# Performance work log

Measured on AMD Instinct MI355X. Metric: run time of the kernel, lower is better.

The kernel has to match this reference:

```python
import jax, jax.numpy as jnp
import numpy as np

EPS = 1e-5
B, C_IN, T_IN = 512, 12, 5000
NF, HID, LAT = 32, 64, 32


def setup_inputs() -> dict:
    key = jax.random.key(0)
    ks = jax.random.split(key, 12)
    inp = {
        "x": jax.random.normal(ks[0], (B, C_IN, T_IN), dtype=jnp.float32),
        # conv stack
        "conv1_w": jax.random.normal(ks[1], (32, C_IN, 50), dtype=jnp.float32) * 0.05,
        "conv1_b": jnp.zeros((32,), dtype=jnp.float32),
        "bn1_g": jnp.ones((32,), dtype=jnp.float32),
        "bn1_b": jnp.zeros((32,), dtype=jnp.float32),
        "conv2_w": jax.random.normal(ks[2], (NF, 32, 25), dtype=jnp.float32) * 0.05,
        "conv2_b": jnp.zeros((NF,), dtype=jnp.float32),
        "bn2_g": jnp.ones((NF,), dtype=jnp.float32),
        "bn2_b": jnp.zeros((NF,), dtype=jnp.float32),
        # input projection + layernorm
        "proj_w": jax.random.normal(ks[3], (LAT, NF), dtype=jnp.float32) * 0.1,
        "proj_b": jnp.zeros((LAT,), dtype=jnp.float32),
        "ln_g": jnp.ones((LAT,), dtype=jnp.float32),
        "ln_b": jnp.zeros((LAT,), dtype=jnp.float32),
        # PLRNN recurrence params
        "A": jnp.eye(LAT, dtype=jnp.float32) * 0.9,
        "W": jax.random.normal(ks[4], (LAT, HID), dtype=jnp.float32) * 0.1,
        "h_bias": jnp.zeros((HID,), dtype=jnp.float32),
        # output projection
        "out_w": jax.random.normal(ks[5], (LAT, LAT), dtype=jnp.float32) * 0.1,
        "out_b": jnp.zeros((LAT,), dtype=jnp.float32),
    }
    return inp


def _conv1d(x, w, b, stride):
    # x: [B, C, T], w: [O, I, K]
    y = jax.lax.conv_general_dilated(
        x, w, window_strides=(stride,), padding="VALID",
        dimension_numbers=("NCH", "OIH", "NCH"))
    return y + b[None, :, None]


def _batchnorm_train(x, g, b):
    # training-mode BN over (batch, time) per channel; x: [B, C, T]
    mean = jnp.mean(x, axis=(0, 2), keepdims=True)
    var = jnp.mean((x - mean) ** 2, axis=(0, 2), keepdims=True)
    return (x - mean) * jax.lax.rsqrt(var + EPS) * g[None, :, None] + b[None, :, None]


def _layernorm(x, g, b):
    mean = jnp.mean(x, axis=-1, keepdims=True)
    var = jnp.mean((x - mean) ** 2, axis=-1, keepdims=True)
    return (x - mean) * jax.lax.rsqrt(var + EPS) * g + b


def reference(x, conv1_w, conv1_b, bn1_g, bn1_b, conv2_w, conv2_b, bn2_g, bn2_b,
              proj_w, proj_b, ln_g, ln_b, A, W, h_bias, out_w, out_b):
    # conv front-end
    y = jax.nn.relu(_batchnorm_train(_conv1d(x, conv1_w, conv1_b, 10), bn1_g, bn1_b))
    y = jax.nn.relu(_batchnorm_train(_conv1d(y, conv2_w, conv2_b, 5), bn2_g, bn2_b))
    y = jnp.transpose(y, (0, 2, 1))  # [B, T, NF], T = 95

    # input projection + LN, vectorized over all timesteps
    xt = _layernorm(jnp.einsum("btf,lf->btl", y, proj_w) + proj_b, ln_g, ln_b)  # [B, T, L]
    xs = jnp.transpose(xt, (1, 0, 2))  # [T, B, L] for scan

    def step(h, x_t):
        # h: [B, L]
        linear = h @ A.T
        nonlinear = jax.nn.relu(h @ W + h_bias) @ W.T
        h_new = linear + nonlinear + x_t
        return h_new, h_new

    h0 = jnp.zeros((x.shape[0], A.shape[0]), dtype=x.dtype)
    _, outputs = jax.lax.scan(step, h0, xs)  # [T, B, L]

    pooled = jnp.mean(outputs, axis=0)  # [B, L]
    return pooled @ out_w.T + out_b
```

## Files before the change

kernel.cpp:

```cpp
#include <hip/hip_runtime.h>

#define NB    512
#define CIN   12
#define TIN   5000
#define C1    32
#define T1    496
#define T2    95
#define LATD  32
#define HIDD  64

#define OFS_STATS 0
#define OFS_W1P   256
#define OFS_W2P   19456
#define OFS_Y1    45056
#define OFS_Y2    8171520
#define OFS_XS    OFS_Y1

__global__ void prep_kernel(const float* __restrict__ w1, const float* __restrict__ w2,
                            float* __restrict__ ws) {
    int idx = blockIdx.x * 256 + threadIdx.x;
    if (idx < 256) ws[idx] = 0.f;
    int j = idx - 256;
    if (j >= 0 && j < 19200) {
        int ic = j / 1600, r = j % 1600, k = r / 32, oc = r % 32;
        ws[OFS_W1P + j] = w1[oc * 600 + ic * 50 + k];
    }
    int j2 = idx - 19456;
    if (j2 >= 0 && j2 < 25600) {
        int ic = j2 / 800, r = j2 % 800, k = r / 32, oc = r % 32;
        ws[OFS_W2P + j2] = w2[oc * 800 + ic * 25 + k];
    }
}

__global__ __launch_bounds__(128, 2) void conv1_kernel(const float* __restrict__ x,
                                                       const float* __restrict__ b1,
                                                       float* __restrict__ ws) {
    const float* w1p = ws + OFS_W1P;
    float* y1 = ws + OFS_Y1;
    float* stats = ws + OFS_STATS;
    int b  = blockIdx.x >> 1;
    int t0 = (blockIdx.x & 1) * 256;
    int tid = threadIdx.x;
    int ocg = tid & 3, tg = tid >> 2;
    int oc0 = ocg * 8, lt0 = tg * 8;
    int xbase = 82 * tg;

    __shared__ __align__(16) float xs_s[2][2664];
    __shared__ __align__(16) float ws_s[2][1600];
    __shared__ float sred[128];

    float acc[8][8];
#pragma unroll
    for (int a = 0; a < 8; ++a)
#pragma unroll
        for (int c = 0; c < 8; ++c) acc[a][c] = 0.f;

    const float* xb = x + (size_t)b * (CIN * TIN) + t0 * 10;
    int nvalid = TIN - t0 * 10;

    float4 px[6];
    float4 pw[4];

    auto fetch = [&](int ic) {
#pragma unroll
        for (int j = 0; j < 6; ++j) {
            int i = tid + j * 128;
            if (i < 650) {
                int src = 4 * i;
                const float* gp = xb + ic * TIN + src;
                float4 v;
                if (src + 4 <= nvalid) {
                    v = *(const float4*)gp;
                } else {
                    v.x = (src + 0 < nvalid) ? gp[0] : 0.f;
                    v.y = (src + 1 < nvalid) ? gp[1] : 0.f;
                    v.z = (src + 2 < nvalid) ? gp[2] : 0.f;
                    v.w = (src + 3 < nvalid) ? gp[3] : 0.f;
                }
                px[j] = v;
            }
        }
#pragma unroll
        for (int j = 0; j < 4; ++j) {
            int i = tid + j * 128;
            if (i < 400) pw[j] = *(const float4*)(w1p + ic * 1600 + 4 * i);
        }
    };

    fetch(0);
    for (int ic = 0; ic < CIN; ++ic) {
        int cur = ic & 1;
        __syncthreads();
#pragma unroll
        for (int j = 0; j < 6; ++j) {
            int i = tid + j * 128;
            if (i < 650) {
                int src = 4 * i;
                int dst = src + (i / 20) * 2;
                float2 lo; lo.x = px[j].x; lo.y = px[j].y;
                float2 hi; hi.x = px[j].z; hi.y = px[j].w;
                *(float2*)&xs_s[cur][dst]     = lo;
                *(float2*)&xs_s[cur][dst + 2] = hi;
            }
        }
#pragma unroll
        for (int j = 0; j < 4; ++j) {
            int i = tid + j * 128;
            if (i < 400) *(float4*)&ws_s[cur][4 * i] = pw[j];
        }
        if (ic + 1 < CIN) fetch(ic + 1);
        __syncthreads();

#pragma unroll 1
        for (int kp = 0; kp < 25; ++kp) {
            const int k = kp * 2;
            const float* wr = &ws_s[cur][k * 32 + oc0];
            float4 w00 = *(const float4*)wr;
            float4 w01 = *(const float4*)(wr + 4);
            float4 w10 = *(const float4*)(wr + 32);
            float4 w11 = *(const float4*)(wr + 36);
            float2 xv[8];
#pragma unroll
            for (int jt = 0; jt < 8; ++jt) {
                int r = jt * 10 + k;
                int ad = xbase + r + ((r >= 80) ? 2 : 0);
                xv[jt] = *(const float2*)&xs_s[cur][ad];
            }
            float wk[8]  = {w00.x, w00.y, w00.z, w00.w, w01.x, w01.y, w01.z, w01.w};
            float wk1[8] = {w10.x, w10.y, w10.z, w10.w, w11.x, w11.y, w11.z, w11.w};
#pragma unroll
            for (int jo = 0; jo < 8; ++jo)
#pragma unroll
                for (int jt = 0; jt < 8; ++jt)
                    acc[jo][jt] = fmaf(wk1[jo], xv[jt].y, fmaf(wk[jo], xv[jt].x, acc[jo][jt]));
        }
    }

    float bias[8];
#pragma unroll
    for (int jo = 0; jo < 8; ++jo) bias[jo] = b1[oc0 + jo];

    bool tvalid = (t0 + lt0) <= (T1 - 8);
    float psum[8], psq[8];
#pragma unroll
    for (int jo = 0; jo < 8; ++jo) {
        float s = 0.f, q = 0.f;
        if (tvalid) {
            float tmp[8];
#pragma unroll
            for (int jt = 0; jt < 8; ++jt) {
                float v = acc[jo][jt] + bias[jo];
                tmp[jt] = v; s += v; q = fmaf(v, v, q);
            }
            float* yrow = y1 + (size_t)(b * 32 + oc0 + jo) * T1 + t0 + lt0;
            float4 o0; o0.x = tmp[0]; o0.y = tmp[1]; o0.z = tmp[2]; o0.w = tmp[3];
            float4 o1; o1.x = tmp[4]; o1.y = tmp[5]; o1.z = tmp[6]; o1.w = tmp[7];
            *(float4*)yrow       = o0;
            *(float4*)(yrow + 4) = o1;
        }
        psum[jo] = s; psq[jo] = q;
    }
#pragma unroll
    for (int off = 32; off >= 4; off >>= 1) {
#pragma unroll
        for (int jo = 0; jo < 8; ++jo) {
            psum[jo] += __shfl_down(psum[jo], off, 64);
            psq[jo]  += __shfl_down(psq[jo],  off, 64);
        }
    }
    int lane = tid & 63, wvi = tid >> 6;
    if (lane < 4) {
#pragma unroll
        for (int jo = 0; jo < 8; ++jo) {
            sred[((wvi * 4 + lane) * 8 + jo) * 2 + 0] = psum[jo];
            sred[((wvi * 4 + lane) * 8 + jo) * 2 + 1] = psq[jo];
        }
    }
    __syncthreads();
    if (tid < 64) {
        int oc = tid >> 1, which = tid & 1;
        int og = oc >> 3, jo = oc & 7;
        float v = sred[((0 * 4 + og) * 8 + jo) * 2 + which] +
                  sred[((1 * 4 + og) * 8 + jo) * 2 + which];
        atomicAdd(&stats[which * 32 + oc], v);
    }
}

__global__ void bnstats_kernel(const float* __restrict__ g, const float* __restrict__ bparm,
                               float* __restrict__ ws, int base_in, int base_out, float invN) {
    int oc = threadIdx.x;
    if (oc < 32) {
        float* stats = ws + OFS_STATS;
        float mean = stats[base_in + oc] * invN;
        float var  = stats[base_in + 32 + oc] * invN - mean * mean;
        float s = g[oc] * rsqrtf(var + 1e-5f);
        stats[base_out + oc]      = s;
        stats[base_out + 32 + oc] = bparm[oc] - mean * s;
    }
}

__global__ __launch_bounds__(192, 2) void conv2_kernel(const float* __restrict__ b2,
                                                       float* __restrict__ ws) {
    const float* w2p = ws + OFS_W2P;
    const float* y1 = ws + OFS_Y1;
    float* y2 = ws + OFS_Y2;
    float* stats = ws + OFS_STATS;
    int b = blockIdx.x;
    int tid = threadIdx.x;
    int ocg = tid & 7, tg = tid >> 3;
    int oc0 = ocg * 4, lt0 = tg * 4;

    __shared__ __align__(16) float a1s[500];
    __shared__ __align__(16) float w2s[800];
    __shared__ float sred[192];

    float acc[4][4];
#pragma unroll
    for (int a = 0; a < 4; ++a)
#pragma unroll
        for (int c = 0; c < 4; ++c) acc[a][c] = 0.f;

    for (int ic = 0; ic < 32; ++ic) {
        __syncthreads();
        float s1  = stats[128 + ic];
        float sh1 = stats[160 + ic];
        const float* yrow = y1 + (size_t)(b * 32 + ic) * T1;
        for (int i = tid; i < 124; i += 192) {
            float4 v = *(const float4*)(yrow + 4 * i);
            v.x = fmaxf(fmaf(v.x, s1, sh1), 0.f);
            v.y = fmaxf(fmaf(v.y, s1, sh1), 0.f);
            v.z = fmaxf(fmaf(v.z, s1, sh1), 0.f);
            v.w = fmaxf(fmaf(v.w, s1, sh1), 0.f);
            *(float4*)&a1s[4 * i] = v;
        }
        for (int i = tid; i < 200; i += 192)
            *(float4*)&w2s[4 * i] = *(const float4*)(w2p + ic * 800 + 4 * i);
        __syncthreads();

#pragma unroll 1
        for (int kp = 0; kp < 12; ++kp) {
            const int k = kp * 2;
            float4 wA = *(const float4*)&w2s[k * 32 + oc0];
            float4 wB = *(const float4*)&w2s[(k + 1) * 32 + oc0];
            float x0[4], x1[4];
#pragma unroll
            for (int jt = 0; jt < 4; ++jt) {
                int a = 20 * tg + 5 * jt + k;
                x0[jt] = a1s[a]; x1[jt] = a1s[a + 1];
            }
            float wk[4]  = {wA.x, wA.y, wA.z, wA.w};
            float wk1[4] = {wB.x, wB.y, wB.z, wB.w};
#pragma unroll
            for (int jo = 0; jo < 4; ++jo)
#pragma unroll
                for (int jt = 0; jt < 4; ++jt)
                    acc[jo][jt] = fmaf(wk1[jo], x1[jt], fmaf(wk[jo], x0[jt], acc[jo][jt]));
        }
        float4 wT = *(const float4*)&w2s[24 * 32 + oc0];
        float wt[4] = {wT.x, wT.y, wT.z, wT.w};
#pragma unroll
        for (int jt = 0; jt < 4; ++jt) {
            float xt_ = a1s[20 * tg + 5 * jt + 24];
#pragma unroll
            for (int jo = 0; jo < 4; ++jo) acc[jo][jt] = fmaf(wt[jo], xt_, acc[jo][jt]);
        }
    }

    float bias[4];
#pragma unroll
    for (int jo = 0; jo < 4; ++jo) bias[jo] = b2[oc0 + jo];

    float psum[4], psq[4];
#pragma unroll
    for (int jo = 0; jo < 4; ++jo) {
        float s = 0.f, q = 0.f;
#pragma unroll
        for (int jt = 0; jt < 4; ++jt) {
            int t2 = lt0 + jt;
            if (t2 < T2) {
                float v = acc[jo][jt] + bias[jo];
                y2[(size_t)(b * 32 + oc0 + jo) * T2 + t2] = v;
                s += v; q = fmaf(v, v, q);
            }
        }
        psum[jo] = s; psq[jo] = q;
    }
#pragma unroll
    for (int off = 32; off >= 8; off >>= 1) {
#pragma unroll
        for (int jo = 0; jo < 4; ++jo) {
            psum[jo] += __shfl_down(psum[jo], off, 64);
            psq[jo]  += __shfl_down(psq[jo],  off, 64);
        }
    }
    int lane = tid & 63, wvi = tid >> 6;
    if (lane < 8) {
#pragma unroll
        for (int jo = 0; jo < 4; ++jo) {
            sred[((wvi * 8 + lane) * 4 + jo) * 2 + 0] = psum[jo];
            sred[((wvi * 8 + lane) * 4 + jo) * 2 + 1] = psq[jo];
        }
    }
    __syncthreads();
    if (tid < 64) {
        int oc = tid >> 1, which = tid & 1;
        int og = oc >> 2, jo = oc & 3;
        float v = 0.f;
#pragma unroll
        for (int w = 0; w < 3; ++w)
            v += sred[((w * 8 + og) * 4 + jo) * 2 + which];
        atomicAdd(&stats[64 + which * 32 + oc], v);
    }
}

__global__ __launch_bounds__(256, 2) void proj_kernel(const float* __restrict__ pw,
                                                      const float* __restrict__ pb,
                                                      const float* __restrict__ lng,
                                                      const float* __restrict__ lnb,
                                                      float* __restrict__ ws) {
    int b = blockIdx.x;
    int tid = threadIdx.x;
    __shared__ float a2s[3040];
    __shared__ float pws[1056];
    const float* stats = ws + OFS_STATS;
    const float* y2 = ws + OFS_Y2 + (size_t)b * (32 * T2);
    float* xsg = ws + OFS_XS;

    for (int f = 0; f < 32; ++f) {
        float s2  = stats[192 + f];
        float sh2 = stats[224 + f];
        if (tid < T2)
            a2s[f * T2 + tid] = fmaxf(fmaf(y2[f * T2 + tid], s2, sh2), 0.f);
    }
    for (int i = tid; i < 1024; i += 256)
        pws[(i >> 5) * 33 + (i & 31)] = pw[i];

    int l = tid & 31, ts = tid >> 5;
    float pbv = pb[l], lg = lng[l], lb = lnb[l];
    __syncthreads();

    for (int it = 0; it < 12; ++it) {
        int t = ts + 8 * it;
        if (t < T2) {
            float v = pbv;
#pragma unroll
            for (int f = 0; f < 32; ++f)
                v = fmaf(a2s[f * T2 + t], pws[l * 33 + f], v);
            float sum = v;
#pragma unroll
            for (int off = 16; off >= 1; off >>= 1) sum += __shfl_xor(sum, off, 64);
            float mean = sum * (1.f / 32.f);
            float d = v - mean;
            float q = d * d;
#pragma unroll
            for (int off = 16; off >= 1; off >>= 1) q += __shfl_xor(q, off, 64);
            float o = d * rsqrtf(q * (1.f / 32.f) + 1e-5f) * lg + lb;
            xsg[(size_t)t * (NB * 32) + b * 32 + l] = o;
        }
    }
}

__global__ __launch_bounds__(64)
__attribute__((amdgpu_waves_per_eu(1, 1)))
void scan_kernel(const float* __restrict__ Am,
                 const float* __restrict__ Wm,
                 const float* __restrict__ hbp,
                 const float* __restrict__ ow,
                 const float* __restrict__ ob,
                 const float* __restrict__ ws,
                 float* __restrict__ out) {
    int b = blockIdx.x;
    int lane = threadIdx.x;
    int l = lane & 31, half = lane >> 5;
    __shared__ __align__(16) float hs[32];
    __shared__ __align__(16) float hds[64];
    __shared__ float ows[1056];

    float Wc[32], WT[32], Ah[16];
#pragma unroll
    for (int j = 0; j < 32; ++j) Wc[j] = Wm[j * HIDD + lane];
#pragma unroll
    for (int m = 0; m < 32; ++m) WT[m] = Wm[l * HIDD + half * 32 + m];
#pragma unroll
    for (int j = 0; j < 16; ++j) Ah[j] = Am[l * 32 + half * 16 + j];
    float hbv = hbp[lane];
    for (int i = lane; i < 1024; i += 64)
        ows[(i >> 5) * 33 + (i & 31)] = ow[i];

    const float* xsg = ws + OFS_XS + b * 32;
    if (lane < 32) hs[l] = 0.f;
    float xv = xsg[l];
    float pool = 0.f;
    __syncthreads();

    for (int t = 0; t < T2; ++t) {
        __syncthreads();
        float4 hv[8];
#pragma unroll
        for (int q = 0; q < 8; ++q) hv[q] = *(const float4*)&hs[4 * q];
        float a0 = hbv, a1 = 0.f, a2 = 0.f, a3 = 0.f;
#pragma unroll
        for (int q = 0; q < 8; ++q) {
            a0 = fmaf(Wc[4 * q + 0], hv[q].x, a0);
            a1 = fmaf(Wc[4 * q + 1], hv[q].y, a1);
            a2 = fmaf(Wc[4 * q + 2], hv[q].z, a2);
            a3 = fmaf(Wc[4 * q + 3], hv[q].w, a3);
        }
        float hid = fmaxf((a0 + a1) + (a2 + a3), 0.f);
        float4 hl[4];
#pragma unroll
        for (int q = 0; q < 4; ++q) hl[q] = *(const float4*)&hs[half * 16 + 4 * q];
        float l0 = 0.f, l1 = 0.f;
#pragma unroll
        for (int q = 0; q < 4; ++q) {
            l0 = fmaf(Ah[4 * q + 0], hl[q].x, l0);
            l1 = fmaf(Ah[4 * q + 1], hl[q].y, l1);
            l0 = fmaf(Ah[4 * q + 2], hl[q].z, l0);
            l1 = fmaf(Ah[4 * q + 3], hl[q].w, l1);
        }
        float lin = l0 + l1;
        hds[lane] = hid;
        __syncthreads();
        float n0 = 0.f, n1 = 0.f, n2 = 0.f, n3 = 0.f;
#pragma unroll
        for (int q = 0; q < 8; ++q) {
            float4 d4 = *(const float4*)&hds[half * 32 + 4 * q];
            n0 = fmaf(WT[4 * q + 0], d4.x, n0);
            n1 = fmaf(WT[4 * q + 1], d4.y, n1);
            n2 = fmaf(WT[4 * q + 2], d4.z, n2);
            n3 = fmaf(WT[4 * q + 3], d4.w, n3);
        }
        float part = (n0 + n1) + (n2 + n3) + lin;
        part += __shfl_xor(part, 32, 64);
        float hnew = part + xv;
        pool += hnew;
        if (t + 1 < T2) xv = xsg[(size_t)(t + 1) * (NB * 32) + l];
        if (lane < 32) hs[l] = hnew;
    }

    __syncthreads();
    if (lane < 32) hs[l] = pool * (1.f / 95.f);
    __syncthreads();
    if (lane < 32) {
        float4 p0 = *(const float4*)&hs[0];
        float4 p1 = *(const float4*)&hs[4];
        float4 p2 = *(const float4*)&hs[8];
        float4 p3 = *(const float4*)&hs[12];
        float4 p4 = *(const float4*)&hs[16];
        float4 p5 = *(const float4*)&hs[20];
        float4 p6 = *(const float4*)&hs[24];
        float4 p7 = *(const float4*)&hs[28];
        float o = ob[l];
        const float* owr = &ows[l * 33];
        o = fmaf(owr[0],  p0.x, o); o = fmaf(owr[1],  p0.y, o);
        o = fmaf(owr[2],  p0.z, o); o = fmaf(owr[3],  p0.w, o);
        o = fmaf(owr[4],  p1.x, o); o = fmaf(owr[5],  p1.y, o);
        o = fmaf(owr[6],  p1.z, o); o = fmaf(owr[7],  p1.w, o);
        o = fmaf(owr[8],  p2.x, o); o = fmaf(owr[9],  p2.y, o);
        o = fmaf(owr[10], p2.z, o); o = fmaf(owr[11], p2.w, o);
        o = fmaf(owr[12], p3.x, o); o = fmaf(owr[13], p3.y, o);
        o = fmaf(owr[14], p3.z, o); o = fmaf(owr[15], p3.w, o);
        o = fmaf(owr[16], p4.x, o); o = fmaf(owr[17], p4.y, o);
        o = fmaf(owr[18], p4.z, o); o = fmaf(owr[19], p4.w, o);
        o = fmaf(owr[20], p5.x, o); o = fmaf(owr[21], p5.y, o);
        o = fmaf(owr[22], p5.z, o); o = fmaf(owr[23], p5.w, o);
        o = fmaf(owr[24], p6.x, o); o = fmaf(owr[25], p6.y, o);
        o = fmaf(owr[26], p6.z, o); o = fmaf(owr[27], p6.w, o);
        o = fmaf(owr[28], p7.x, o); o = fmaf(owr[29], p7.y, o);
        o = fmaf(owr[30], p7.z, o); o = fmaf(owr[31], p7.w, o);
        out[b * 32 + l] = o;
    }
}

extern "C" void kernel_launch(void* const* d_in, const int* in_sizes, int n_in,
                              void* d_out, int out_size, void* d_ws, size_t ws_size,
                              hipStream_t stream) {
    (void)in_sizes; (void)n_in; (void)out_size; (void)ws_size;
    const float* x   = (const float*)d_in[0];
    const float* w1  = (const float*)d_in[1];
    const float* b1  = (const float*)d_in[2];
    const float* g1  = (const float*)d_in[3];
    const float* be1 = (const float*)d_in[4];
    const float* w2  = (const float*)d_in[5];
    const float* b2  = (const float*)d_in[6];
    const float* g2  = (const float*)d_in[7];
    const float* be2 = (const float*)d_in[8];
    const float* pw  = (const float*)d_in[9];
    const float* pb  = (const float*)d_in[10];
    const float* lng = (const float*)d_in[11];
    const float* lnb = (const float*)d_in[12];
    const float* Am  = (const float*)d_in[13];
    const float* Wm  = (const float*)d_in[14];
    const float* hb  = (const float*)d_in[15];
    const float* ow  = (const float*)d_in[16];
    const float* ob  = (const float*)d_in[17];
    float* ws  = (float*)d_ws;
    float* out = (float*)d_out;

    prep_kernel<<<176, 256, 0, stream>>>(w1, w2, ws);
    conv1_kernel<<<1024, 128, 0, stream>>>(x, b1, ws);
    bnstats_kernel<<<1, 64, 0, stream>>>(g1, be1, ws, 0, 128, 1.f / 253952.f);
    conv2_kernel<<<512, 192, 0, stream>>>(b2, ws);
    bnstats_kernel<<<1, 64, 0, stream>>>(g2, be2, ws, 64, 192, 1.f / 48640.f);
    proj_kernel<<<512, 256, 0, stream>>>(pw, pb, lng, lnb, ws);
    scan_kernel<<<512, 64, 0, stream>>>(Am, Wm, hb, ow, ob, ws, out);
}
```

Before: 468.6 us.

## Fuse BN stats, proj and scan kernels; async LDS loads in conv1

Moves the conv1 input and weight staging to global_load_lds async copies with a new time-interleaved layout, so each thread handles strided timesteps instead of contiguous ones. Folds the BN1 finalize into conv2 and pipelines conv2 with register prefetch at 256 threads. Fuses the BN2 finalize, the projection+layernorm and the recurrent scan into one kernel that keeps the projected inputs in LDS instead of a global [T,B,L] buffer. This cuts launches and global round trips. The trade-offs are only 64 of 256 threads doing the serial scan, and the LDS barriers in the scan loop are removed.

```diff
diff --git a/kernel.cpp b/kernel.cpp
--- a/kernel.cpp
+++ b/kernel.cpp
@@ -1,20 +1,22 @@
 #include <hip/hip_runtime.h>
+#include <stdint.h>
 
 #define NB    512
 #define CIN   12
 #define TIN   5000
-#define C1    32
 #define T1    496
 #define T2    95
-#define LATD  32
-#define HIDD  64
 
 #define OFS_STATS 0
 #define OFS_W1P   256
 #define OFS_W2P   19456
 #define OFS_Y1    45056
 #define OFS_Y2    8171520
-#define OFS_XS    OFS_Y1
+
+#define GAS __attribute__((address_space(1)))
+#define LAS __attribute__((address_space(3)))
+#define ASYNC_COPY16(gp, lp) \
+    __builtin_amdgcn_global_load_lds((const GAS void*)(gp), (LAS void*)(lp), 16, 0, 0)
 
 __global__ void prep_kernel(const float* __restrict__ w1, const float* __restrict__ w2,
                             float* __restrict__ ws) {
@@ -42,10 +44,10 @@
     int t0 = (blockIdx.x & 1) * 256;
     int tid = threadIdx.x;
     int ocg = tid & 3, tg = tid >> 2;
-    int oc0 = ocg * 8, lt0 = tg * 8;
-    int xbase = 82 * tg;
-
-    __shared__ __align__(16) float xs_s[2][2664];
+    int oc0 = ocg * 8;
+    int xoff = 10 * tg;
+
+    __shared__ __align__(16) float xs_s[2][2600];
     __shared__ __align__(16) float ws_s[2][1600];
     __shared__ float sred[128];
 
@@ -56,83 +58,62 @@
         for (int c = 0; c < 8; ++c) acc[a][c] = 0.f;
 
     const float* xb = x + (size_t)b * (CIN * TIN) + t0 * 10;
-    int nvalid = TIN - t0 * 10;
-
-    float4 px[6];
-    float4 pw[4];
-
-    auto fetch = [&](int ic) {
-#pragma unroll
-        for (int j = 0; j < 6; ++j) {
-            int i = tid + j * 128;
-            if (i < 650) {
-                int src = 4 * i;
-                const float* gp = xb + ic * TIN + src;
-                float4 v;
-                if (src + 4 <= nvalid) {
-                    v = *(const float4*)gp;
-                } else {
-                    v.x = (src + 0 < nvalid) ? gp[0] : 0.f;
-                    v.y = (src + 1 < nvalid) ? gp[1] : 0.f;
-                    v.z = (src + 2 < nvalid) ? gp[2] : 0.f;
-                    v.w = (src + 3 < nvalid) ? gp[3] : 0.f;
-                }
-                px[j] = v;
-            }
-        }
-#pragma unroll
-        for (int j = 0; j < 4; ++j) {
-            int i = tid + j * 128;
-            if (i < 400) pw[j] = *(const float4*)(w1p + ic * 1600 + 4 * i);
+    const int nchunk = (t0 == 0) ? 650 : 610;
+    const int wbase = tid & ~63;
+
+    if (t0 != 0) {
+        for (int i = tid; i < 160; i += 128) {
+            xs_s[0][2440 + i] = 0.f;
+            xs_s[1][2440 + i] = 0.f;
+        }
+    }
+
+    auto issue = [&](int ic) {
+        int buf = ic & 1;
+        const float* xg = xb + ic * TIN;
+#pragma unroll
+        for (int c = 0; c < 6; ++c) {
+            int i = c * 128 + tid;
+            if (i < nchunk)
+                ASYNC_COPY16(xg + 4 * i, &xs_s[buf][4 * (c * 128 + wbase)]);
+        }
+        const float* wg = w1p + ic * 1600;
+#pragma unroll
+        for (int c = 0; c < 4; ++c) {
+            int i = c * 128 + tid;
+            if (i < 400)
+                ASYNC_COPY16(wg + 4 * i, &ws_s[buf][4 * (c * 128 + wbase)]);
         }
     };
 
-    fetch(0);
+    issue(0);
     for (int ic = 0; ic < CIN; ++ic) {
-        int cur = ic & 1;
+        const int cur = ic & 1;
         __syncthreads();
-#pragma unroll
-        for (int j = 0; j < 6; ++j) {
-            int i = tid + j * 128;
-            if (i < 650) {
-                int src = 4 * i;
-                int dst = src + (i / 20) * 2;
-                float2 lo; lo.x = px[j].x; lo.y = px[j].y;
-                float2 hi; hi.x = px[j].z; hi.y = px[j].w;
-                *(float2*)&xs_s[cur][dst]     = lo;
-                *(float2*)&xs_s[cur][dst + 2] = hi;
-            }
-        }
-#pragma unroll
-        for (int j = 0; j < 4; ++j) {
-            int i = tid + j * 128;
-            if (i < 400) *(float4*)&ws_s[cur][4 * i] = pw[j];
-        }
-        if (ic + 1 < CIN) fetch(ic + 1);
-        __syncthreads();
+        if (ic + 1 < CIN) issue(ic + 1);
 
 #pragma unroll 1
-        for (int kp = 0; kp < 25; ++kp) {
-            const int k = kp * 2;
-            const float* wr = &ws_s[cur][k * 32 + oc0];
-            float4 w00 = *(const float4*)wr;
-            float4 w01 = *(const float4*)(wr + 4);
-            float4 w10 = *(const float4*)(wr + 32);
-            float4 w11 = *(const float4*)(wr + 36);
-            float2 xv[8];
-#pragma unroll
-            for (int jt = 0; jt < 8; ++jt) {
-                int r = jt * 10 + k;
-                int ad = xbase + r + ((r >= 80) ? 2 : 0);
-                xv[jt] = *(const float2*)&xs_s[cur][ad];
-            }
-            float wk[8]  = {w00.x, w00.y, w00.z, w00.w, w01.x, w01.y, w01.z, w01.w};
-            float wk1[8] = {w10.x, w10.y, w10.z, w10.w, w11.x, w11.y, w11.z, w11.w};
-#pragma unroll
-            for (int jo = 0; jo < 8; ++jo)
-#pragma unroll
-                for (int jt = 0; jt < 8; ++jt)
-                    acc[jo][jt] = fmaf(wk1[jo], xv[jt].y, fmaf(wk[jo], xv[jt].x, acc[jo][jt]));
+        for (int m = 0; m < 5; ++m) {
+#pragma unroll
+            for (int u = 0; u < 5; ++u) {
+                const int k = m * 10 + u * 2;
+                const float* wr = &ws_s[cur][k * 32 + oc0];
+                float4 w00 = *(const float4*)(wr);
+                float4 w01 = *(const float4*)(wr + 4);
+                float4 w10 = *(const float4*)(wr + 32);
+                float4 w11 = *(const float4*)(wr + 36);
+                float2 xv[8];
+#pragma unroll
+                for (int j = 0; j < 8; ++j)
+                    xv[j] = *(const float2*)&xs_s[cur][xoff + 320 * j + k];
+                float wk[8]  = {w00.x, w00.y, w00.z, w00.w, w01.x, w01.y, w01.z, w01.w};
+                float wk1[8] = {w10.x, w10.y, w10.z, w10.w, w11.x, w11.y, w11.z, w11.w};
+#pragma unroll
+                for (int jo = 0; jo < 8; ++jo)
+#pragma unroll
+                    for (int j = 0; j < 8; ++j)
+                        acc[jo][j] = fmaf(wk1[jo], xv[j].y, fmaf(wk[jo], xv[j].x, acc[jo][j]));
+            }
         }
     }
 
@@ -140,25 +121,22 @@
 #pragma unroll
     for (int jo = 0; jo < 8; ++jo) bias[jo] = b1[oc0 + jo];
 
-    bool tvalid = (t0 + lt0) <= (T1 - 8);
     float psum[8], psq[8];
 #pragma unroll
+    for (int jo = 0; jo < 8; ++jo) { psum[jo] = 0.f; psq[jo] = 0.f; }
+#pragma unroll
     for (int jo = 0; jo < 8; ++jo) {
-        float s = 0.f, q = 0.f;
-        if (tvalid) {
-            float tmp[8];
-#pragma unroll
-            for (int jt = 0; jt < 8; ++jt) {
-                float v = acc[jo][jt] + bias[jo];
-                tmp[jt] = v; s += v; q = fmaf(v, v, q);
-            }
-            float* yrow = y1 + (size_t)(b * 32 + oc0 + jo) * T1 + t0 + lt0;
-            float4 o0; o0.x = tmp[0]; o0.y = tmp[1]; o0.z = tmp[2]; o0.w = tmp[3];
-            float4 o1; o1.x = tmp[4]; o1.y = tmp[5]; o1.z = tmp[6]; o1.w = tmp[7];
-            *(float4*)yrow       = o0;
-            *(float4*)(yrow + 4) = o1;
-        }
-        psum[jo] = s; psq[jo] = q;
+        float* yrow = y1 + (size_t)(b * 32 + oc0 + jo) * T1 + t0 + tg;
+#pragma unroll
+        for (int j = 0; j < 8; ++j) {
+            int trel = tg + 32 * j;
+            if (t0 + trel < T1) {
+                float v = acc[jo][j] + bias[jo];
+                yrow[32 * j] = v;
+                psum[jo] += v;
+                psq[jo] = fmaf(v, v, psq[jo]);
+            }
+        }
     }
 #pragma unroll
     for (int off = 32; off >= 4; off >>= 1) {
@@ -186,66 +164,70 @@
     }
 }
 
-__global__ void bnstats_kernel(const float* __restrict__ g, const float* __restrict__ bparm,
-                               float* __restrict__ ws, int base_in, int base_out, float invN) {
-    int oc = threadIdx.x;
-    if (oc < 32) {
-        float* stats = ws + OFS_STATS;
-        float mean = stats[base_in + oc] * invN;
-        float var  = stats[base_in + 32 + oc] * invN - mean * mean;
-        float s = g[oc] * rsqrtf(var + 1e-5f);
-        stats[base_out + oc]      = s;
-        stats[base_out + 32 + oc] = bparm[oc] - mean * s;
-    }
-}
-
-__global__ __launch_bounds__(192, 2) void conv2_kernel(const float* __restrict__ b2,
-                                                       float* __restrict__ ws) {
+__global__ __launch_bounds__(256, 2) void conv2bn_kernel(const float* __restrict__ g1,
+                                                         const float* __restrict__ be1,
+                                                         const float* __restrict__ b2,
+                                                         float* __restrict__ ws) {
     const float* w2p = ws + OFS_W2P;
     const float* y1 = ws + OFS_Y1;
     float* y2 = ws + OFS_Y2;
     float* stats = ws + OFS_STATS;
-    int b = blockIdx.x;
-    int tid = threadIdx.x;
+    int b = blockIdx.x, tid = threadIdx.x;
     int ocg = tid & 7, tg = tid >> 3;
-    int oc0 = ocg * 4, lt0 = tg * 4;
-
-    __shared__ __align__(16) float a1s[500];
+    int oc0 = ocg * 4;
+
+    __shared__ float s1s[32], sh1s[32];
+    __shared__ __align__(16) float a1s[512];
     __shared__ __align__(16) float w2s[800];
-    __shared__ float sred[192];
-
-    float acc[4][4];
+    __shared__ float sred[256];
+
+    float acc[4][3];
 #pragma unroll
     for (int a = 0; a < 4; ++a)
 #pragma unroll
-        for (int c = 0; c < 4; ++c) acc[a][c] = 0.f;
-
+        for (int c = 0; c < 3; ++c) acc[a][c] = 0.f;
+
+    if (tid < 32) {
+        float mean = stats[tid] * (1.f / 253952.f);
+        float var  = stats[32 + tid] * (1.f / 253952.f) - mean * mean;
+        float s = g1[tid] * rsqrtf(var + 1e-5f);
+        s1s[tid] = s;
+        sh1s[tid] = be1[tid] - mean * s;
+    }
+
+    float4 pa, pw2;
+    auto fetch = [&](int ic) {
+        if (tid < 124) pa  = *(const float4*)(y1 + (size_t)(b * 32 + ic) * T1 + 4 * tid);
+        if (tid < 200) pw2 = *(const float4*)(w2p + ic * 800 + 4 * tid);
+    };
+    fetch(0);
+    __syncthreads();
+
+#pragma unroll 1
     for (int ic = 0; ic < 32; ++ic) {
-        __syncthreads();
-        float s1  = stats[128 + ic];
-        float sh1 = stats[160 + ic];
-        const float* yrow = y1 + (size_t)(b * 32 + ic) * T1;
-        for (int i = tid; i < 124; i += 192) {
-            float4 v = *(const float4*)(yrow + 4 * i);
+        float s1 = s1s[ic], sh1 = sh1s[ic];
+        if (tid < 124) {
+            float4 v = pa;
             v.x = fmaxf(fmaf(v.x, s1, sh1), 0.f);
             v.y = fmaxf(fmaf(v.y, s1, sh1), 0.f);
             v.z = fmaxf(fmaf(v.z, s1, sh1), 0.f);
             v.w = fmaxf(fmaf(v.w, s1, sh1), 0.f);
-            *(float4*)&a1s[4 * i] = v;
-        }
-        for (int i = tid; i < 200; i += 192)
-            *(float4*)&w2s[4 * i] = *(const float4*)(w2p + ic * 800 + 4 * i);
+            *(float4*)&a1s[4 * tid] = v;
+        }
+        if (tid < 200) *(float4*)&w2s[4 * tid] = pw2;
+        if (ic + 1 < 32) fetch(ic + 1);
+        __builtin_amdgcn_sched_barrier(0);
         __syncthreads();
 
-#pragma unroll 1
+#pragma unroll
         for (int kp = 0; kp < 12; ++kp) {
             const int k = kp * 2;
             float4 wA = *(const float4*)&w2s[k * 32 + oc0];
             float4 wB = *(const float4*)&w2s[(k + 1) * 32 + oc0];
-            float x0[4], x1[4];
-#pragma unroll
-            for (int jt = 0; jt < 4; ++jt) {
-                int a = 20 * tg + 5 * jt + k;
+            float x0[3], x1[3];
+#pragma unroll
+            for (int jt = 0; jt < 3; ++jt) {
+                int a = 15 * tg + 5 * jt + k;
                 x0[jt] = a1s[a]; x1[jt] = a1s[a + 1];
             }
             float wk[4]  = {wA.x, wA.y, wA.z, wA.w};
@@ -253,17 +235,20 @@
 #pragma unroll
             for (int jo = 0; jo < 4; ++jo)
 #pragma unroll
-                for (int jt = 0; jt < 4; ++jt)
+                for (int jt = 0; jt < 3; ++jt)
                     acc[jo][jt] = fmaf(wk1[jo], x1[jt], fmaf(wk[jo], x0[jt], acc[jo][jt]));
         }
-        float4 wT = *(const float4*)&w2s[24 * 32 + oc0];
-        float wt[4] = {wT.x, wT.y, wT.z, wT.w};
-#pragma unroll
-        for (int jt = 0; jt < 4; ++jt) {
-            float xt_ = a1s[20 * tg + 5 * jt + 24];
-#pragma unroll
-            for (int jo = 0; jo < 4; ++jo) acc[jo][jt] = fmaf(wt[jo], xt_, acc[jo][jt]);
-        }
+        {
+            float4 wT = *(const float4*)&w2s[24 * 32 + oc0];
+            float wt[4] = {wT.x, wT.y, wT.z, wT.w};
+#pragma unroll
+            for (int jt = 0; jt < 3; ++jt) {
+                float xt_ = a1s[15 * tg + 5 * jt + 24];
+#pragma unroll
+                for (int jo = 0; jo < 4; ++jo) acc[jo][jt] = fmaf(wt[jo], xt_, acc[jo][jt]);
+            }
+        }
+        __syncthreads();
     }
 
     float bias[4];
@@ -275,11 +260,11 @@
     for (int jo = 0; jo < 4; ++jo) {
         float s = 0.f, q = 0.f;
 #pragma unroll
-        for (int jt = 0; jt < 4; ++jt) {
-            int t2 = lt0 + jt;
+        for (int jt = 0; jt < 3; ++jt) {
+            int t2 = 3 * tg + jt;
             if (t2 < T2) {
                 float v = acc[jo][jt] + bias[jo];
-                y2[(size_t)(b * 32 + oc0 + jo) * T2 + t2] = v;
+                y2[(size_t)b * 3040 + (oc0 + jo) * T2 + t2] = v;
                 s += v; q = fmaf(v, v, q);
             }
         }
@@ -307,168 +292,175 @@
         int og = oc >> 2, jo = oc & 3;
         float v = 0.f;
 #pragma unroll
-        for (int w = 0; w < 3; ++w)
+        for (int w = 0; w < 4; ++w)
             v += sred[((w * 8 + og) * 4 + jo) * 2 + which];
         atomicAdd(&stats[64 + which * 32 + oc], v);
     }
 }
 
-__global__ __launch_bounds__(256, 2) void proj_kernel(const float* __restrict__ pw,
-                                                      const float* __restrict__ pb,
-                                                      const float* __restrict__ lng,
-                                                      const float* __restrict__ lnb,
-                                                      float* __restrict__ ws) {
-    int b = blockIdx.x;
-    int tid = threadIdx.x;
-    __shared__ float a2s[3040];
-    __shared__ float pws[1056];
-    const float* stats = ws + OFS_STATS;
-    const float* y2 = ws + OFS_Y2 + (size_t)b * (32 * T2);
-    float* xsg = ws + OFS_XS;
-
-    for (int f = 0; f < 32; ++f) {
-        float s2  = stats[192 + f];
-        float sh2 = stats[224 + f];
-        if (tid < T2)
-            a2s[f * T2 + tid] = fmaxf(fmaf(y2[f * T2 + tid], s2, sh2), 0.f);
-    }
-    for (int i = tid; i < 1024; i += 256)
-        pws[(i >> 5) * 33 + (i & 31)] = pw[i];
-
-    int l = tid & 31, ts = tid >> 5;
-    float pbv = pb[l], lg = lng[l], lb = lnb[l];
-    __syncthreads();
-
-    for (int it = 0; it < 12; ++it) {
-        int t = ts + 8 * it;
-        if (t < T2) {
-            float v = pbv;
-#pragma unroll
-            for (int f = 0; f < 32; ++f)
-                v = fmaf(a2s[f * T2 + t], pws[l * 33 + f], v);
-            float sum = v;
-#pragma unroll
-            for (int off = 16; off >= 1; off >>= 1) sum += __shfl_xor(sum, off, 64);
-            float mean = sum * (1.f / 32.f);
-            float d = v - mean;
-            float q = d * d;
-#pragma unroll
-            for (int off = 16; off >= 1; off >>= 1) q += __shfl_xor(q, off, 64);
-            float o = d * rsqrtf(q * (1.f / 32.f) + 1e-5f) * lg + lb;
-            xsg[(size_t)t * (NB * 32) + b * 32 + l] = o;
-        }
-    }
-}
-
-__global__ __launch_bounds__(64)
-__attribute__((amdgpu_waves_per_eu(1, 1)))
-void scan_kernel(const float* __restrict__ Am,
-                 const float* __restrict__ Wm,
-                 const float* __restrict__ hbp,
-                 const float* __restrict__ ow,
-                 const float* __restrict__ ob,
-                 const float* __restrict__ ws,
-                 float* __restrict__ out) {
-    int b = blockIdx.x;
-    int lane = threadIdx.x;
-    int l = lane & 31, half = lane >> 5;
+__global__ __launch_bounds__(256, 2) void projscan_kernel(const float* __restrict__ g2,
+                                                          const float* __restrict__ be2,
+                                                          const float* __restrict__ pw,
+                                                          const float* __restrict__ pb,
+                                                          const float* __restrict__ lng,
+                                                          const float* __restrict__ lnb,
+                                                          const float* __restrict__ Am,
+                                                          const float* __restrict__ Wm,
+                                                          const float* __restrict__ hbp,
+                                                          const float* __restrict__ ow,
+                                                          const float* __restrict__ ob,
+                                                          const float* __restrict__ ws,
+                                                          float* __restrict__ out) {
+    int b = blockIdx.x, tid = threadIdx.x;
+    __shared__ float s2s[32], sh2s[32];
+    __shared__ __align__(16) float a2s[3040];
+    __shared__ float pws[1056], ows[1056];
+    __shared__ __align__(16) float xsl[3135];
     __shared__ __align__(16) float hs[32];
     __shared__ __align__(16) float hds[64];
-    __shared__ float ows[1056];
-
-    float Wc[32], WT[32], Ah[16];
-#pragma unroll
-    for (int j = 0; j < 32; ++j) Wc[j] = Wm[j * HIDD + lane];
-#pragma unroll
-    for (int m = 0; m < 32; ++m) WT[m] = Wm[l * HIDD + half * 32 + m];
-#pragma unroll
-    for (int j = 0; j < 16; ++j) Ah[j] = Am[l * 32 + half * 16 + j];
-    float hbv = hbp[lane];
-    for (int i = lane; i < 1024; i += 64)
+    const float* stats = ws + OFS_STATS;
+    const float* y2b = ws + OFS_Y2 + (size_t)b * 3040;
+
+    if (tid < 32) {
+        float mean = stats[64 + tid] * (1.f / 48640.f);
+        float var  = stats[96 + tid] * (1.f / 48640.f) - mean * mean;
+        float s = g2[tid] * rsqrtf(var + 1e-5f);
+        s2s[tid] = s;
+        sh2s[tid] = be2[tid] - mean * s;
+    }
+    for (int i = tid; i < 1024; i += 256) {
+        pws[(i >> 5) * 33 + (i & 31)] = pw[i];
         ows[(i >> 5) * 33 + (i & 31)] = ow[i];
-
-    const float* xsg = ws + OFS_XS + b * 32;
-    if (lane < 32) hs[l] = 0.f;
-    float xv = xsg[l];
-    float pool = 0.f;
-    __syncthreads();
-
-    for (int t = 0; t < T2; ++t) {
-        __syncthreads();
-        float4 hv[8];
-#pragma unroll
-        for (int q = 0; q < 8; ++q) hv[q] = *(const float4*)&hs[4 * q];
-        float a0 = hbv, a1 = 0.f, a2 = 0.f, a3 = 0.f;
-#pragma unroll
-        for (int q = 0; q < 8; ++q) {
-            a0 = fmaf(Wc[4 * q + 0], hv[q].x, a0);
-            a1 = fmaf(Wc[4 * q + 1], hv[q].y, a1);
-            a2 = fmaf(Wc[4 * q + 2], hv[q].z, a2);
-            a3 = fmaf(Wc[4 * q + 3], hv[q].w, a3);
-        }
-        float hid = fmaxf((a0 + a1) + (a2 + a3), 0.f);
-        float4 hl[4];
-#pragma unroll
-        for (int q = 0; q < 4; ++q) hl[q] = *(const float4*)&hs[half * 16 + 4 * q];
-        float l0 = 0.f, l1 = 0.f;
-#pragma unroll
-        for (int q = 0; q < 4; ++q) {
-            l0 = fmaf(Ah[4 * q + 0], hl[q].x, l0);
-            l1 = fmaf(Ah[4 * q + 1], hl[q].y, l1);
-            l0 = fmaf(Ah[4 * q + 2], hl[q].z, l0);
-            l1 = fmaf(Ah[4 * q + 3], hl[q].w, l1);
-        }
-        float lin = l0 + l1;
-        hds[lane] = hid;
-        __syncthreads();
-        float n0 = 0.f, n1 = 0.f, n2 = 0.f, n3 = 0.f;
-#pragma unroll
-        for (int q = 0; q < 8; ++q) {
-            float4 d4 = *(const float4*)&hds[half * 32 + 4 * q];
-            n0 = fmaf(WT[4 * q + 0], d4.x, n0);
-            n1 = fmaf(WT[4 * q + 1], d4.y, n1);
-            n2 = fmaf(WT[4 * q + 2], d4.z, n2);
-            n3 = fmaf(WT[4 * q + 3], d4.w, n3);
-        }
-        float part = (n0 + n1) + (n2 + n3) + lin;
-        part += __shfl_xor(part, 32, 64);
-        float hnew = part + xv;
-        pool += hnew;
-        if (t + 1 < T2) xv = xsg[(size_t)(t + 1) * (NB * 32) + l];
-        if (lane < 32) hs[l] = hnew;
-    }
-
-    __syncthreads();
-    if (lane < 32) hs[l] = pool * (1.f / 95.f);
-    __syncthreads();
-    if (lane < 32) {
-        float4 p0 = *(const float4*)&hs[0];
-        float4 p1 = *(const float4*)&hs[4];
-        float4 p2 = *(const float4*)&hs[8];
-        float4 p3 = *(const float4*)&hs[12];
-        float4 p4 = *(const float4*)&hs[16];
-        float4 p5 = *(const float4*)&hs[20];
-        float4 p6 = *(const float4*)&hs[24];
-        float4 p7 = *(const float4*)&hs[28];
-        float o = ob[l];
-        const float* owr = &ows[l * 33];
-        o = fmaf(owr[0],  p0.x, o); o = fmaf(owr[1],  p0.y, o);
-        o = fmaf(owr[2],  p0.z, o); o = fmaf(owr[3],  p0.w, o);
-        o = fmaf(owr[4],  p1.x, o); o = fmaf(owr[5],  p1.y, o);
-        o = fmaf(owr[6],  p1.z, o); o = fmaf(owr[7],  p1.w, o);
-        o = fmaf(owr[8],  p2.x, o); o = fmaf(owr[9],  p2.y, o);
-        o = fmaf(owr[10], p2.z, o); o = fmaf(owr[11], p2.w, o);
-        o = fmaf(owr[12], p3.x, o); o = fmaf(owr[13], p3.y, o);
-        o = fmaf(owr[14], p3.z, o); o = fmaf(owr[15], p3.w, o);
-        o = fmaf(owr[16], p4.x, o); o = fmaf(owr[17], p4.y, o);
-        o = fmaf(owr[18], p4.z, o); o = fmaf(owr[19], p4.w, o);
-        o = fmaf(owr[20], p5.x, o); o = fmaf(owr[21], p5.y, o);
-        o = fmaf(owr[22], p5.z, o); o = fmaf(owr[23], p5.w, o);
-        o = fmaf(owr[24], p6.x, o); o = fmaf(owr[25], p6.y, o);
-        o = fmaf(owr[26], p6.z, o); o = fmaf(owr[27], p6.w, o);
-        o = fmaf(owr[28], p7.x, o); o = fmaf(owr[29], p7.y, o);
-        o = fmaf(owr[30], p7.z, o); o = fmaf(owr[31], p7.w, o);
-        out[b * 32 + l] = o;
+    }
+    __syncthreads();
+
+    for (int i = tid; i < 760; i += 256) {
+        float4 v = *(const float4*)(y2b + 4 * i);
+        float r[4] = {v.x, v.y, v.z, v.w};
+        float o[4];
+#pragma unroll
+        for (int e = 0; e < 4; ++e) {
+            int idx = 4 * i + e;
+            int oc = idx / 95;
+            o[e] = fmaxf(fmaf(r[e], s2s[oc], sh2s[oc]), 0.f);
+        }
+        float4 vv; vv.x = o[0]; vv.y = o[1]; vv.z = o[2]; vv.w = o[3];
+        *(float4*)&a2s[4 * i] = vv;
+    }
+    __syncthreads();
+
+    int l = tid & 31, ts = tid >> 5;
+    {
+        float pbv = pb[l], lg = lng[l], lb = lnb[l];
+        for (int it = 0; it < 12; ++it) {
+            int t = ts + 8 * it;
+            if (t < T2) {
+                float v = pbv;
+#pragma unroll
+                for (int f = 0; f < 32; ++f)
+                    v = fmaf(a2s[f * T2 + t], pws[l * 33 + f], v);
+                float sum = v;
+#pragma unroll
+                for (int off = 16; off >= 1; off >>= 1) sum += __shfl_xor(sum, off, 64);
+                float mean = sum * (1.f / 32.f);
+                float d = v - mean;
+                float q = d * d;
+#pragma unroll
+                for (int off = 16; off >= 1; off >>= 1) q += __shfl_xor(q, off, 64);
+                float o = d * rsqrtf(q * (1.f / 32.f) + 1e-5f) * lg + lb;
+                xsl[t * 33 + l] = o;
+            }
+        }
+    }
+    __syncthreads();
+
+    if (tid < 64) {
+        int lane = tid, half = lane >> 5;
+        float Wc[32], WT[32], Ah[16];
+#pragma unroll
+        for (int j = 0; j < 32; ++j) Wc[j] = Wm[j * 64 + lane];
+#pragma unroll
+        for (int m = 0; m < 32; ++m) WT[m] = Wm[l * 64 + half * 32 + m];
+#pragma unroll
+        for (int j = 0; j < 16; ++j) Ah[j] = Am[l * 32 + half * 16 + j];
+        float hbv = hbp[lane];
+        if (lane < 32) hs[l] = 0.f;
+        float xv = xsl[l];
+        float pool = 0.f;
+
+        for (int t = 0; t < T2; ++t) {
+            float4 hv[8];
+#pragma unroll
+            for (int q = 0; q < 8; ++q) hv[q] = *(const float4*)&hs[4 * q];
+            float a0 = hbv, a1 = 0.f, a2 = 0.f, a3 = 0.f;
+#pragma unroll
+            for (int q = 0; q < 8; ++q) {
+                a0 = fmaf(Wc[4 * q + 0], hv[q].x, a0);
+                a1 = fmaf(Wc[4 * q + 1], hv[q].y, a1);
+                a2 = fmaf(Wc[4 * q + 2], hv[q].z, a2);
+                a3 = fmaf(Wc[4 * q + 3], hv[q].w, a3);
+            }
+            float hid = fmaxf((a0 + a1) + (a2 + a3), 0.f);
+            float4 hl[4];
+#pragma unroll
+            for (int q = 0; q < 4; ++q) hl[q] = *(const float4*)&hs[half * 16 + 4 * q];
+            float l0 = 0.f, l1 = 0.f;
+#pragma unroll
+            for (int q = 0; q < 4; ++q) {
+                l0 = fmaf(Ah[4 * q + 0], hl[q].x, l0);
+                l1 = fmaf(Ah[4 * q + 1], hl[q].y, l1);
+                l0 = fmaf(Ah[4 * q + 2], hl[q].z, l0);
+                l1 = fmaf(Ah[4 * q + 3], hl[q].w, l1);
+            }
+            float lin = l0 + l1;
+            hds[lane] = hid;
+            float n0 = 0.f, n1 = 0.f, n2 = 0.f, n3 = 0.f;
+#pragma unroll
+            for (int q = 0; q < 8; ++q) {
+                float4 d4 = *(const float4*)&hds[half * 32 + 4 * q];
+                n0 = fmaf(WT[4 * q + 0], d4.x, n0);
+                n1 = fmaf(WT[4 * q + 1], d4.y, n1);
+                n2 = fmaf(WT[4 * q + 2], d4.z, n2);
+                n3 = fmaf(WT[4 * q + 3], d4.w, n3);
+            }
+            float part = (n0 + n1) + (n2 + n3) + lin;
+            part += __shfl_xor(part, 32, 64);
+            float hnew = part + xv;
+            pool += hnew;
+            if (t + 1 < T2) xv = xsl[(t + 1) * 33 + l];
+            if (lane < 32) hs[l] = hnew;
+        }
+
+        if (lane < 32) hs[l] = pool * (1.f / 95.f);
+        if (lane < 32) {
+            float4 p0 = *(const float4*)&hs[0];
+            float4 p1 = *(const float4*)&hs[4];
+            float4 p2 = *(const float4*)&hs[8];
+            float4 p3 = *(const float4*)&hs[12];
+            float4 p4 = *(const float4*)&hs[16];
+            float4 p5 = *(const float4*)&hs[20];
+            float4 p6 = *(const float4*)&hs[24];
+            float4 p7 = *(const float4*)&hs[28];
+            float o = ob[l];
+            const float* owr = &ows[l * 33];
+            o = fmaf(owr[0],  p0.x, o); o = fmaf(owr[1],  p0.y, o);
+            o = fmaf(owr[2],  p0.z, o); o = fmaf(owr[3],  p0.w, o);
+            o = fmaf(owr[4],  p1.x, o); o = fmaf(owr[5],  p1.y, o);
+            o = fmaf(owr[6],  p1.z, o); o = fmaf(owr[7],  p1.w, o);
+            o = fmaf(owr[8],  p2.x, o); o = fmaf(owr[9],  p2.y, o);
+            o = fmaf(owr[10], p2.z, o); o = fmaf(owr[11], p2.w, o);
+            o = fmaf(owr[12], p3.x, o); o = fmaf(owr[13], p3.y, o);
+            o = fmaf(owr[14], p3.z, o); o = fmaf(owr[15], p3.w, o);
+            o = fmaf(owr[16], p4.x, o); o = fmaf(owr[17], p4.y, o);
+            o = fmaf(owr[18], p4.z, o); o = fmaf(owr[19], p4.w, o);
+            o = fmaf(owr[20], p5.x, o); o = fmaf(owr[21], p5.y, o);
+            o = fmaf(owr[22], p5.z, o); o = fmaf(owr[23], p5.w, o);
+            o = fmaf(owr[24], p6.x, o); o = fmaf(owr[25], p6.y, o);
+            o = fmaf(owr[26], p6.z, o); o = fmaf(owr[27], p6.w, o);
+            o = fmaf(owr[28], p7.x, o); o = fmaf(owr[29], p7.y, o);
+            o = fmaf(owr[30], p7.z, o); o = fmaf(owr[31], p7.w, o);
+            out[b * 32 + l] = o;
+        }
     }
 }
 
@@ -499,9 +491,7 @@
 
     prep_kernel<<<176, 256, 0, stream>>>(w1, w2, ws);
     conv1_kernel<<<1024, 128, 0, stream>>>(x, b1, ws);
-    bnstats_kernel<<<1, 64, 0, stream>>>(g1, be1, ws, 0, 128, 1.f / 253952.f);
-    conv2_kernel<<<512, 192, 0, stream>>>(b2, ws);
-    bnstats_kernel<<<1, 64, 0, stream>>>(g2, be2, ws, 64, 192, 1.f / 48640.f);
-    proj_kernel<<<512, 256, 0, stream>>>(pw, pb, lng, lnb, ws);
-    scan_kernel<<<512, 64, 0, stream>>>(Am, Wm, hb, ow, ob, ws, out);
+    conv2bn_kernel<<<512, 256, 0, stream>>>(g1, be1, b2, ws);
+    projscan_kernel<<<512, 256, 0, stream>>>(g2, be2, pw, pb, lng, lnb,
+                                             Am, Wm, hb, ow, ob, ws, out);
 }
```

After: 498.8 us. 1.06x slower.
